# Kernel tuning notes

Measured on AMD Instinct MI355X. Metric: run time of the kernel, lower is better.

The kernel has to match this reference:

```python
import jax, jax.numpy as jnp
import numpy as np

N_NODES = 100000
N_EDGES = 3200000
N_FEAT = 128
N_GRAPHS = 64


def setup_inputs() -> dict:
    key = jax.random.key(0)
    ks = jax.random.split(key, 8)
    x = jax.random.normal(ks[0], (N_NODES, N_FEAT), dtype=jnp.float32)
    edge_index = jax.random.randint(ks[1], (2, N_EDGES), 0, N_NODES, dtype=jnp.int64)
    batch = jnp.sort(jax.random.randint(ks[2], (N_NODES,), 0, N_GRAPHS, dtype=jnp.int64))
    # GCNConv weights (glorot-style scale) and biases
    W1 = jax.random.normal(ks[3], (N_FEAT, 32), dtype=jnp.float32) / np.sqrt(N_FEAT)
    b1 = jnp.zeros((32,), dtype=jnp.float32)
    W2 = jax.random.normal(ks[4], (32, 16), dtype=jnp.float32) / np.sqrt(32.0)
    b2 = jnp.zeros((16,), dtype=jnp.float32)
    lin_w = jax.random.normal(ks[5], (16, 1), dtype=jnp.float32) / np.sqrt(16.0)
    lin_b = jnp.zeros((1,), dtype=jnp.float32)
    return {"x": x, "edge_index": edge_index, "batch": batch,
            "W1": W1, "b1": b1, "W2": W2, "b2": b2,
            "lin_w": lin_w, "lin_b": lin_b}


def _gcn_conv(x, W, b, src, dst, deg_inv_sqrt, n_nodes):
    # transform first (fewer features downstream when out_dim < in_dim)
    xw = x @ W  # [N, out]
    norm = deg_inv_sqrt[src] * deg_inv_sqrt[dst]  # [E+N]
    msg = xw[src] * norm[:, None]  # gather + scale
    out = jax.ops.segment_sum(msg, dst, num_segments=n_nodes)  # scatter-add
    return out + b


def reference(x, edge_index, batch, W1, b1, W2, b2, lin_w, lin_b):
    n_nodes = x.shape[0]
    self_loop = jnp.arange(n_nodes, dtype=edge_index.dtype)
    src = jnp.concatenate([edge_index[0], self_loop])
    dst = jnp.concatenate([edge_index[1], self_loop])
    # symmetric GCN normalization with self-loops
    deg = jax.ops.segment_sum(jnp.ones_like(src, dtype=x.dtype), dst,
                              num_segments=n_nodes)
    deg_inv_sqrt = jnp.where(deg > 0, jax.lax.rsqrt(jnp.maximum(deg, 1.0)), 0.0)

    h = _gcn_conv(x, W1, b1, src, dst, deg_inv_sqrt, n_nodes)
    h = jax.nn.relu(h)
    # F.dropout with training=False (eval) is identity
    h = _gcn_conv(h, W2, b2, src, dst, deg_inv_sqrt, n_nodes)

    # global_mean_pool over batch index
    sums = jax.ops.segment_sum(h, batch, num_segments=N_GRAPHS)  # [G,16]
    cnts = jax.ops.segment_sum(jnp.ones((n_nodes,), dtype=h.dtype), batch,
                               num_segments=N_GRAPHS)
    pooled = sums / jnp.maximum(cnts, 1.0)[:, None]
    return pooled @ lin_w + lin_b  # [G,1]
```

## Files before the change

### kernel.cpp

```cpp
#include <hip/hip_runtime.h>

#define NN 100000
#define NE 3200000
#define NF 128
#define C1 32
#define C2 16
#define NG 64
#define BKT_SH 7
#define BKT_W  128
#define NBKT   782
#define CH     8192
#define NW     391
#define RSTR   784
#define MAPCAP 6400

#define OFF_BCNT  0
#define OFF_CNTF  2048
#define OFF_RUN   2304
#define OFF_ROW   308848
#define OFF_DIS   408864
#define OFF_EDG   508864
#define OFF_XS2B  (OFF_EDG + NE)
#define OFF_COL   (OFF_XS2B + NN*8)
#define OFF_XS1   (OFF_COL + NE)

__device__ __forceinline__ unsigned pack_bf2(float a, float b) {
    unsigned ua = __float_as_uint(a);
    unsigned ub = __float_as_uint(b);
    ua = (ua + 0x7fffu + ((ua >> 16) & 1u)) >> 16;
    ub = (ub + 0x7fffu + ((ub >> 16) & 1u)) & 0xffff0000u;
    return ua | ub;
}
__device__ __forceinline__ float2 unpack_bf2(unsigned u) {
    return make_float2(__uint_as_float(u << 16), __uint_as_float(u & 0xffff0000u));
}
__device__ __forceinline__ void acc4(float4& a, uint2 q) {
    float2 f0 = unpack_bf2(q.x), f1 = unpack_bf2(q.y);
    a.x += f0.x; a.y += f0.y; a.z += f1.x; a.w += f1.y;
}

__global__ __launch_bounds__(512) void k_part(
    const int* __restrict__ S, const int* __restrict__ D,
    unsigned* __restrict__ edgebuf, int* __restrict__ runstart,
    int* __restrict__ bcnt)
{
    __shared__ int lhist[1024];
    __shared__ int lstart[1024];
    __shared__ int lcur[NBKT];
    __shared__ int wsum[8];
    __shared__ unsigned lsort[CH];
    const int w = blockIdx.x;
    const int t = threadIdx.x;
    const int e0 = w * CH;
    const int n = min(CH, NE - e0);
    const int n4 = n >> 2;
    const int4* __restrict__ S4 = (const int4*)(S + e0);
    const int4* __restrict__ D4 = (const int4*)(D + e0);

    for (int i = t; i < 1024; i += 512) lhist[i] = 0;
    __syncthreads();
    for (int i = t; i < n4; i += 512) {
        int4 d = D4[i];
        atomicAdd(&lhist[(unsigned)d.x >> BKT_SH], 1);
        atomicAdd(&lhist[(unsigned)d.y >> BKT_SH], 1);
        atomicAdd(&lhist[(unsigned)d.z >> BKT_SH], 1);
        atomicAdd(&lhist[(unsigned)d.w >> BKT_SH], 1);
    }
    __syncthreads();
    for (int i = t; i < NBKT; i += 512) atomicAdd(&bcnt[i], lhist[i]);

    int c0 = lhist[t * 2 + 0], c1 = lhist[t * 2 + 1];
    int ts = c0 + c1;
    const int lane = t & 63, wv = t >> 6;
    int sc = ts;
    #pragma unroll
    for (int off = 1; off < 64; off <<= 1) {
        int v = __shfl_up(sc, off, 64);
        if (lane >= off) sc += v;
    }
    if (lane == 63) wsum[wv] = sc;
    __syncthreads();
    int wo = 0;
    #pragma unroll
    for (int i = 0; i < 8; ++i) wo += (i < wv) ? wsum[i] : 0;
    int excl = sc - ts + wo;
    lstart[t * 2 + 0] = excl;
    lstart[t * 2 + 1] = excl + c0;
    __syncthreads();

    for (int i = t; i < 783; i += 512) runstart[w * RSTR + i] = lstart[i];
    for (int i = t; i < NBKT; i += 512) lcur[i] = lstart[i];
    __syncthreads();
    for (int i = t; i < n4; i += 512) {
        int4 s = S4[i];
        int4 d = D4[i];
        { int p = atomicAdd(&lcur[(unsigned)d.x >> BKT_SH], 1);
          lsort[p] = ((unsigned)s.x << BKT_SH) | ((unsigned)d.x & (BKT_W - 1)); }
        { int p = atomicAdd(&lcur[(unsigned)d.y >> BKT_SH], 1);
          lsort[p] = ((unsigned)s.y << BKT_SH) | ((unsigned)d.y & (BKT_W - 1)); }
        { int p = atomicAdd(&lcur[(unsigned)d.z >> BKT_SH], 1);
          lsort[p] = ((unsigned)s.z << BKT_SH) | ((unsigned)d.z & (BKT_W - 1)); }
        { int p = atomicAdd(&lcur[(unsigned)d.w >> BKT_SH], 1);
          lsort[p] = ((unsigned)s.w << BKT_SH) | ((unsigned)d.w & (BKT_W - 1)); }
    }
    __syncthreads();
    {
        uint4* __restrict__ eb4 = (uint4*)(edgebuf + e0);
        const uint4* __restrict__ ls4 = (const uint4*)lsort;
        for (int i = t; i < n4; i += 512) eb4[i] = ls4[i];
    }
}

union FGShare {
    struct { unsigned short map[MAPCAP]; unsigned ebuf[MAPCAP]; } f;
    struct { float xls[128 * 33]; float wls[32 * 32]; } g;
};

__global__ __launch_bounds__(256) void k_fillgemm(
    const unsigned* __restrict__ edgebuf, const int* __restrict__ runstart,
    const int* __restrict__ bcnt, const int* __restrict__ batch,
    int* __restrict__ rowstart, float* __restrict__ dis, int* __restrict__ colidx,
    float* __restrict__ cntf,
    const float* __restrict__ x, const float* __restrict__ W1,
    unsigned* __restrict__ xs1)
{
    __shared__ FGShare u;
    __shared__ int rl[NW];
    __shared__ int pfx[NW];
    __shared__ int basea[NW];
    __shared__ int lcnt[BKT_W];
    __shared__ int lcur[BKT_W];
    __shared__ float dloc[BKT_W];
    __shared__ float gcnt[NG];
    __shared__ int wsum[4];
    __shared__ int hs1;
    const int b = blockIdx.x;
    const int t = threadIdx.x;
    const int lane = t & 63, wv = t >> 6;

    if (t < NG) gcnt[t] = 0.f;

    int accp = 0;
    for (int i = t; i < b; i += 256) accp += bcnt[i];
    #pragma unroll
    for (int off = 1; off < 64; off <<= 1) accp += __shfl_xor(accp, off, 64);
    if (lane == 0) wsum[wv] = accp;

    for (int w = t; w < NW; w += 256) {
        int s0 = runstart[w * RSTR + b];
        int s1 = runstart[w * RSTR + b + 1];
        basea[w] = s0;
        rl[w] = s1 - s0;
    }
    if (t < BKT_W) lcnt[t] = 0;
    __syncthreads();
    const int bs = wsum[0] + wsum[1] + wsum[2] + wsum[3];

    int w0 = t * 2;
    int c0 = (w0 < NW) ? rl[w0] : 0;
    int c1 = (w0 + 1 < NW) ? rl[w0 + 1] : 0;
    int ts = c0 + c1;
    int sc = ts;
    #pragma unroll
    for (int off = 1; off < 64; off <<= 1) {
        int v = __shfl_up(sc, off, 64);
        if (lane >= off) sc += v;
    }
    __syncthreads();
    if (lane == 63) wsum[wv] = sc;
    __syncthreads();
    int wo = 0;
    #pragma unroll
    for (int i = 0; i < 4; ++i) wo += (i < wv) ? wsum[i] : 0;
    const int total = wsum[0] + wsum[1] + wsum[2] + wsum[3];
    int excl0 = sc - ts + wo;
    if (w0 < NW)     pfx[w0]     = excl0;
    if (w0 + 1 < NW) pfx[w0 + 1] = excl0 + c0;
    __syncthreads();

    for (int w = t; w < NW; w += 256) {
        int p = pfx[w], len = rl[w];
        basea[w] = w * CH + basea[w] - p;
        for (int i = 0; i < len; ++i) u.f.map[p + i] = (unsigned short)w;
    }
    __syncthreads();
    for (int j = t; j < total; j += 256) {
        unsigned p = edgebuf[basea[u.f.map[j]] + j];
        u.f.ebuf[j] = p;
        atomicAdd(&lcnt[p & (BKT_W - 1)], 1);
    }
    __syncthreads();

    int myc = 0, sc2 = 0;
    if (t < BKT_W) {
        myc = lcnt[t];
        sc2 = myc;
        #pragma unroll
        for (int off = 1; off < 64; off <<= 1) {
            int v = __shfl_up(sc2, off, 64);
            if (lane >= off) sc2 += v;
        }
        if (t == 63) hs1 = sc2;
    }
    __syncthreads();
    if (t < BKT_W) {
        int excl = sc2 - myc + ((t >= 64) ? hs1 : 0);
        int node = b * BKT_W + t;
        float dv = rsqrtf((float)myc + 1.0f);
        dloc[t] = dv;
        if (node < NN) {
            rowstart[node] = bs + excl;
            dis[node] = dv;
            atomicAdd(&gcnt[batch[node]], 1.0f);
        }
        lcur[t] = bs + excl;
    }
    if (b == 0 && t == 0) rowstart[NN] = NE;
    __syncthreads();
    for (int j = t; j < total; j += 256) {
        unsigned p = u.f.ebuf[j];
        int pos = atomicAdd(&lcur[p & (BKT_W - 1)], 1);
        colidx[pos] = (int)(p >> BKT_SH);
    }
    __syncthreads();
    if (t < NG && gcnt[t] != 0.f) atomicAdd(&cntf[t], gcnt[t]);

    const int tc = t & 7;
    const int tr = t >> 3;
    const int base = b * 128;
    float a[4][4] = {};

    for (int k0 = 0; k0 < NF; k0 += 32) {
        {
            int i = t * 4;
            int kk = i >> 5, c = i & 31;
            *(float4*)&u.g.wls[kk * 32 + c] = *(const float4*)&W1[(k0 + kk) * C1 + c];
        }
        #pragma unroll
        for (int r = 0; r < 4; ++r) {
            int n = (t >> 3) + r * 32;
            int j = (t & 7) * 4;
            int node = base + n;
            float4 v = make_float4(0.f, 0.f, 0.f, 0.f);
            if (node < NN) v = *(const float4*)&x[(long long)node * NF + k0 + j];
            u.g.xls[n * 33 + j + 0] = v.x;
            u.g.xls[n * 33 + j + 1] = v.y;
            u.g.xls[n * 33 + j + 2] = v.z;
            u.g.xls[n * 33 + j + 3] = v.w;
        }
        __syncthreads();
        #pragma unroll 8
        for (int kk = 0; kk < 32; ++kk) {
            float4 w = *(const float4*)&u.g.wls[kk * 32 + tc * 4];
            #pragma unroll
            for (int i = 0; i < 4; ++i) {
                float xv = u.g.xls[(tr * 4 + i) * 33 + kk];
                a[i][0] = fmaf(xv, w.x, a[i][0]);
                a[i][1] = fmaf(xv, w.y, a[i][1]);
                a[i][2] = fmaf(xv, w.z, a[i][2]);
                a[i][3] = fmaf(xv, w.w, a[i][3]);
            }
        }
        __syncthreads();
    }
    #pragma unroll
    for (int i = 0; i < 4; ++i) {
        int node = base + tr * 4 + i;
        if (node < NN) {
            float dv = dloc[tr * 4 + i];
            uint2 o;
            o.x = pack_bf2(a[i][0] * dv, a[i][1] * dv);
            o.y = pack_bf2(a[i][2] * dv, a[i][3] * dv);
            *(uint2*)&xs1[node * 16 + tc * 2] = o;
        }
    }
}

__global__ __launch_bounds__(256) void k_gather1(
    const unsigned* __restrict__ xs1, const int* __restrict__ colidx,
    const int* __restrict__ rowstart, const float* __restrict__ dis,
    const float* __restrict__ b1, const float* __restrict__ W2,
    const float* __restrict__ b2, const float* __restrict__ lw,
    const float* __restrict__ lb, float* __restrict__ out,
    unsigned* __restrict__ xs2b)
{
    __shared__ float w2s[C1 * C2];
    __shared__ float hrow[32 * 33];
    const int t = threadIdx.x;
    if (t < 128) *(float4*)&w2s[t * 4] = *(const float4*)&W2[t * 4];
    if (blockIdx.x == 0 && t < NG) {
        float s = lb[0];
        #pragma unroll
        for (int k = 0; k < C2; ++k) s = fmaf(b2[k], lw[k], s);
        out[t] = s;
    }
    const int l = t & 7;
    const int n = t >> 3;
    const int v = blockIdx.x * 32 + n;

    const int start = rowstart[v];
    const int num = rowstart[v + 1] - start;
    const int* __restrict__ cp = &colidx[start];
    const uint2* __restrict__ tb = (const uint2*)xs1;
    float4 a0 = make_float4(0.f, 0.f, 0.f, 0.f);
    float4 a1 = a0, a2 = a0, a3 = a0;
    acc4(a0, tb[v * 8 + l]);
    int i = 0;
    if (num >= 8) {
        int idx[8];
        #pragma unroll
        for (int j = 0; j < 8; ++j) idx[j] = cp[j];
        for (; i + 16 <= num; i += 8) {
            int nx[8];
            #pragma unroll
            for (int j = 0; j < 8; ++j) nx[j] = cp[i + 8 + j];
            uint2 q[8];
            #pragma unroll
            for (int j = 0; j < 8; ++j) q[j] = tb[idx[j] * 8 + l];
            acc4(a0, q[0]); acc4(a1, q[1]); acc4(a2, q[2]); acc4(a3, q[3]);
            acc4(a0, q[4]); acc4(a1, q[5]); acc4(a2, q[6]); acc4(a3, q[7]);
            #pragma unroll
            for (int j = 0; j < 8; ++j) idx[j] = nx[j];
        }
        {
            uint2 q[8];
            #pragma unroll
            for (int j = 0; j < 8; ++j) q[j] = tb[idx[j] * 8 + l];
            acc4(a0, q[0]); acc4(a1, q[1]); acc4(a2, q[2]); acc4(a3, q[3]);
            acc4(a0, q[4]); acc4(a1, q[5]); acc4(a2, q[6]); acc4(a3, q[7]);
            i += 8;
        }
    }
    for (; i < num; ++i) acc4(a0, tb[cp[i] * 8 + l]);
    float ax = (a0.x + a1.x) + (a2.x + a3.x);
    float ay = (a0.y + a1.y) + (a2.y + a3.y);
    float az = (a0.z + a1.z) + (a2.z + a3.z);
    float aw = (a0.w + a1.w) + (a2.w + a3.w);
    const float dv = dis[v];

    hrow[n * 33 + l * 4 + 0] = fmaxf(fmaf(ax, dv, b1[l * 4 + 0]), 0.f);
    hrow[n * 33 + l * 4 + 1] = fmaxf(fmaf(ay, dv, b1[l * 4 + 1]), 0.f);
    hrow[n * 33 + l * 4 + 2] = fmaxf(fmaf(az, dv, b1[l * 4 + 2]), 0.f);
    hrow[n * 33 + l * 4 + 3] = fmaxf(fmaf(aw, dv, b1[l * 4 + 3]), 0.f);
    __syncthreads();

    const float* hr = &hrow[n * 33];
    float s0 = 0.f, s1 = 0.f;
    #pragma unroll
    for (int k = 0; k < 32; ++k) {
        float hv = hr[k];
        s0 = fmaf(hv, w2s[k * C2 + 2 * l + 0], s0);
        s1 = fmaf(hv, w2s[k * C2 + 2 * l + 1], s1);
    }
    xs2b[v * 8 + l] = pack_bf2(s0 * dv, s1 * dv);
}

__global__ __launch_bounds__(256) void k_gather2(
    const unsigned* __restrict__ xs2b, const int* __restrict__ colidx,
    const int* __restrict__ rowstart, const float* __restrict__ dis,
    const int* __restrict__ batch, const float* __restrict__ cntf,
    const float* __restrict__ lw, float* __restrict__ out)
{
    __shared__ float sg[NG];
    const int t = threadIdx.x;
    if (t < NG) sg[t] = 0.f;
    __syncthreads();

    const int l = t & 3;
    const int n = t >> 2;
    const int v = blockIdx.x * 64 + n;
    const bool valid = v < NN;

    float4 r = make_float4(0.f, 0.f, 0.f, 0.f);
    int g = 0;
    if (valid) {
        const int start = rowstart[v];
        const int num = rowstart[v + 1] - start;
        const int* __restrict__ cp = &colidx[start];
        const uint2* __restrict__ tb = (const uint2*)xs2b;
        float4 a0 = make_float4(0.f, 0.f, 0.f, 0.f);
        float4 a1 = a0, a2 = a0, a3 = a0;
        acc4(a0, tb[v * 4 + l]);
        int i = 0;
        if (num >= 8) {
            int idx[8];
            #pragma unroll
            for (int j = 0; j < 8; ++j) idx[j] = cp[j];
            for (; i + 16 <= num; i += 8) {
                int nx[8];
                #pragma unroll
                for (int j = 0; j < 8; ++j) nx[j] = cp[i + 8 + j];
                uint2 q[8];
                #pragma unroll
                for (int j = 0; j < 8; ++j) q[j] = tb[idx[j] * 4 + l];
                acc4(a0, q[0]); acc4(a1, q[1]); acc4(a2, q[2]); acc4(a3, q[3]);
                acc4(a0, q[4]); acc4(a1, q[5]); acc4(a2, q[6]); acc4(a3, q[7]);
                #pragma unroll
                for (int j = 0; j < 8; ++j) idx[j] = nx[j];
            }
            {
                uint2 q[8];
                #pragma unroll
                for (int j = 0; j < 8; ++j) q[j] = tb[idx[j] * 4 + l];
                acc4(a0, q[0]); acc4(a1, q[1]); acc4(a2, q[2]); acc4(a3, q[3]);
                acc4(a0, q[4]); acc4(a1, q[5]); acc4(a2, q[6]); acc4(a3, q[7]);
                i += 8;
            }
        }
        for (; i < num; ++i) acc4(a0, tb[cp[i] * 4 + l]);
        float dv = dis[v];
        g = batch[v];
        r.x = ((a0.x + a1.x) + (a2.x + a3.x)) * dv;
        r.y = ((a0.y + a1.y) + (a2.y + a3.y)) * dv;
        r.z = ((a0.z + a1.z) + (a2.z + a3.z)) * dv;
        r.w = ((a0.w + a1.w) + (a2.w + a3.w)) * dv;
    }

    float part = r.x * lw[l * 4 + 0] + r.y * lw[l * 4 + 1]
               + r.z * lw[l * 4 + 2] + r.w * lw[l * 4 + 3];
    part += __shfl_xor(part, 1, 64);
    part += __shfl_xor(part, 2, 64);
    if (valid && l == 0) {
        float c = fmaxf(cntf[g], 1.0f);
        atomicAdd(&sg[g], part / c);
    }
    __syncthreads();
    if (t < NG && sg[t] != 0.f) atomicAdd(&out[t], sg[t]);
}

extern "C" void kernel_launch(void* const* d_in, const int* in_sizes, int n_in,
                              void* d_out, int out_size, void* d_ws, size_t ws_size,
                              hipStream_t stream) {
    const float* x     = (const float*)d_in[0];
    const int*   ei    = (const int*)d_in[1];
    const int*   batch = (const int*)d_in[2];
    const float* W1    = (const float*)d_in[3];
    const float* b1    = (const float*)d_in[4];
    const float* W2    = (const float*)d_in[5];
    const float* b2    = (const float*)d_in[6];
    const float* lw    = (const float*)d_in[7];
    const float* lb    = (const float*)d_in[8];
    float* out = (float*)d_out;

    float*    wsf = (float*)d_ws;
    int*      wsi = (int*)d_ws;
    unsigned* wsu = (unsigned*)d_ws;

    int*      bcnt     = wsi + OFF_BCNT;
    float*    cntf     = wsf + OFF_CNTF;
    int*      runstart = wsi + OFF_RUN;
    int*      rowstart = wsi + OFF_ROW;
    float*    dis      = wsf + OFF_DIS;
    unsigned* edgebuf  = wsu + OFF_EDG;
    unsigned* xs1      = wsu + OFF_XS1;
    unsigned* xs2b     = wsu + OFF_XS2B;
    int*      colidx   = wsi + OFF_COL;

    const int* S = ei;
    const int* D = ei + NE;

    hipMemsetAsync(wsi + OFF_BCNT, 0, 2304 * sizeof(int), stream);

    k_part       <<<NW, 512, 0, stream>>>(S, D, edgebuf, runstart, bcnt);
    k_fillgemm   <<<NBKT, 256, 0, stream>>>(edgebuf, runstart, bcnt, batch,
                                            rowstart, dis, colidx, cntf, x, W1, xs1);
    k_gather1    <<<NN / 32, 256, 0, stream>>>(xs1, colidx, rowstart, dis, b1, W2,
                                               b2, lw, lb, out, xs2b);
    k_gather2    <<<(NN + 63) / 64, 256, 0, stream>>>(xs2b, colidx, rowstart, dis,
                                                      batch, cntf, lw, out);
}
```

Before: 251.5 us.

## Replace two-pass bucket partition CSR build with global atomic counting sort

Drops the shared-memory bucket partition and per-bucket fill in favour of a plain counting sort: a global-atomic degree histogram, a row-offset prefix computed inside the GEMM kernel, and a scatter kernel that places source indices with global atomics on per-node cursors. This removes the intermediate edge buffer and the run-start bookkeeping. In exchange it issues 6.4M global atomics to random addresses and writes colidx scattered, and the neighbour order within a row is no longer deterministic.

```diff
diff --git a/kernel.cpp b/kernel.cpp
--- a/kernel.cpp
+++ b/kernel.cpp
@@ -6,23 +6,17 @@
 #define C1 32
 #define C2 16
 #define NG 64
-#define BKT_SH 7
 #define BKT_W  128
 #define NBKT   782
-#define CH     8192
-#define NW     391
-#define RSTR   784
-#define MAPCAP 6400
-
-#define OFF_BCNT  0
-#define OFF_CNTF  2048
-#define OFF_RUN   2304
-#define OFF_ROW   308848
-#define OFF_DIS   408864
-#define OFF_EDG   508864
-#define OFF_XS2B  (OFF_EDG + NE)
-#define OFF_COL   (OFF_XS2B + NN*8)
-#define OFF_XS1   (OFF_COL + NE)
+
+#define OFF_CNTF  0
+#define OFF_DEG   64
+#define OFF_ROW   100160
+#define OFF_CUR   200176
+#define OFF_DIS   300176
+#define OFF_COL   400176
+#define OFF_XS1   3600176
+#define OFF_XS2B  5200176
 
 __device__ __forceinline__ unsigned pack_bf2(float a, float b) {
     unsigned ua = __float_as_uint(a);
@@ -39,97 +33,28 @@
     a.x += f0.x; a.y += f0.y; a.z += f1.x; a.w += f1.y;
 }
 
-__global__ __launch_bounds__(512) void k_part(
-    const int* __restrict__ S, const int* __restrict__ D,
-    unsigned* __restrict__ edgebuf, int* __restrict__ runstart,
-    int* __restrict__ bcnt)
-{
-    __shared__ int lhist[1024];
-    __shared__ int lstart[1024];
-    __shared__ int lcur[NBKT];
-    __shared__ int wsum[8];
-    __shared__ unsigned lsort[CH];
-    const int w = blockIdx.x;
-    const int t = threadIdx.x;
-    const int e0 = w * CH;
-    const int n = min(CH, NE - e0);
-    const int n4 = n >> 2;
-    const int4* __restrict__ S4 = (const int4*)(S + e0);
-    const int4* __restrict__ D4 = (const int4*)(D + e0);
-
-    for (int i = t; i < 1024; i += 512) lhist[i] = 0;
-    __syncthreads();
-    for (int i = t; i < n4; i += 512) {
-        int4 d = D4[i];
-        atomicAdd(&lhist[(unsigned)d.x >> BKT_SH], 1);
-        atomicAdd(&lhist[(unsigned)d.y >> BKT_SH], 1);
-        atomicAdd(&lhist[(unsigned)d.z >> BKT_SH], 1);
-        atomicAdd(&lhist[(unsigned)d.w >> BKT_SH], 1);
-    }
-    __syncthreads();
-    for (int i = t; i < NBKT; i += 512) atomicAdd(&bcnt[i], lhist[i]);
-
-    int c0 = lhist[t * 2 + 0], c1 = lhist[t * 2 + 1];
-    int ts = c0 + c1;
-    const int lane = t & 63, wv = t >> 6;
-    int sc = ts;
-    #pragma unroll
-    for (int off = 1; off < 64; off <<= 1) {
-        int v = __shfl_up(sc, off, 64);
-        if (lane >= off) sc += v;
-    }
-    if (lane == 63) wsum[wv] = sc;
-    __syncthreads();
-    int wo = 0;
-    #pragma unroll
-    for (int i = 0; i < 8; ++i) wo += (i < wv) ? wsum[i] : 0;
-    int excl = sc - ts + wo;
-    lstart[t * 2 + 0] = excl;
-    lstart[t * 2 + 1] = excl + c0;
-    __syncthreads();
-
-    for (int i = t; i < 783; i += 512) runstart[w * RSTR + i] = lstart[i];
-    for (int i = t; i < NBKT; i += 512) lcur[i] = lstart[i];
-    __syncthreads();
-    for (int i = t; i < n4; i += 512) {
-        int4 s = S4[i];
-        int4 d = D4[i];
-        { int p = atomicAdd(&lcur[(unsigned)d.x >> BKT_SH], 1);
-          lsort[p] = ((unsigned)s.x << BKT_SH) | ((unsigned)d.x & (BKT_W - 1)); }
-        { int p = atomicAdd(&lcur[(unsigned)d.y >> BKT_SH], 1);
-          lsort[p] = ((unsigned)s.y << BKT_SH) | ((unsigned)d.y & (BKT_W - 1)); }
-        { int p = atomicAdd(&lcur[(unsigned)d.z >> BKT_SH], 1);
-          lsort[p] = ((unsigned)s.z << BKT_SH) | ((unsigned)d.z & (BKT_W - 1)); }
-        { int p = atomicAdd(&lcur[(unsigned)d.w >> BKT_SH], 1);
-          lsort[p] = ((unsigned)s.w << BKT_SH) | ((unsigned)d.w & (BKT_W - 1)); }
-    }
-    __syncthreads();
-    {
-        uint4* __restrict__ eb4 = (uint4*)(edgebuf + e0);
-        const uint4* __restrict__ ls4 = (const uint4*)lsort;
-        for (int i = t; i < n4; i += 512) eb4[i] = ls4[i];
-    }
-}
-
-union FGShare {
-    struct { unsigned short map[MAPCAP]; unsigned ebuf[MAPCAP]; } f;
-    struct { float xls[128 * 33]; float wls[32 * 32]; } g;
-};
-
-__global__ __launch_bounds__(256) void k_fillgemm(
-    const unsigned* __restrict__ edgebuf, const int* __restrict__ runstart,
-    const int* __restrict__ bcnt, const int* __restrict__ batch,
-    int* __restrict__ rowstart, float* __restrict__ dis, int* __restrict__ colidx,
+__global__ __launch_bounds__(512) void k_deg(
+    const int* __restrict__ D, int* __restrict__ deg)
+{
+    int i = blockIdx.x * 512 + threadIdx.x;
+    if (i < NE / 4) {
+        int4 d = ((const int4*)D)[i];
+        atomicAdd(&deg[d.x], 1);
+        atomicAdd(&deg[d.y], 1);
+        atomicAdd(&deg[d.z], 1);
+        atomicAdd(&deg[d.w], 1);
+    }
+}
+
+__global__ __launch_bounds__(256) void k_rowsgemm(
+    const int* __restrict__ deg, const int* __restrict__ batch,
+    int* __restrict__ rowstart, int* __restrict__ cur, float* __restrict__ dis,
     float* __restrict__ cntf,
     const float* __restrict__ x, const float* __restrict__ W1,
     unsigned* __restrict__ xs1)
 {
-    __shared__ FGShare u;
-    __shared__ int rl[NW];
-    __shared__ int pfx[NW];
-    __shared__ int basea[NW];
-    __shared__ int lcnt[BKT_W];
-    __shared__ int lcur[BKT_W];
+    __shared__ float xls[128 * 33];
+    __shared__ float wls[32 * 32];
     __shared__ float dloc[BKT_W];
     __shared__ float gcnt[NG];
     __shared__ int wsum[4];
@@ -140,61 +65,27 @@
 
     if (t < NG) gcnt[t] = 0.f;
 
-    int accp = 0;
-    for (int i = t; i < b; i += 256) accp += bcnt[i];
+    int acc = 0;
+    {
+        const int lim4 = (b * BKT_W) >> 2;
+        const int4* dg4 = (const int4*)deg;
+        for (int i = t; i < lim4; i += 256) {
+            int4 q = dg4[i];
+            acc += (q.x + q.y) + (q.z + q.w);
+        }
+    }
     #pragma unroll
-    for (int off = 1; off < 64; off <<= 1) accp += __shfl_xor(accp, off, 64);
-    if (lane == 0) wsum[wv] = accp;
-
-    for (int w = t; w < NW; w += 256) {
-        int s0 = runstart[w * RSTR + b];
-        int s1 = runstart[w * RSTR + b + 1];
-        basea[w] = s0;
-        rl[w] = s1 - s0;
-    }
-    if (t < BKT_W) lcnt[t] = 0;
+    for (int off = 1; off < 64; off <<= 1) acc += __shfl_xor(acc, off, 64);
+    if (lane == 0) wsum[wv] = acc;
     __syncthreads();
     const int bs = wsum[0] + wsum[1] + wsum[2] + wsum[3];
 
-    int w0 = t * 2;
-    int c0 = (w0 < NW) ? rl[w0] : 0;
-    int c1 = (w0 + 1 < NW) ? rl[w0 + 1] : 0;
-    int ts = c0 + c1;
-    int sc = ts;
-    #pragma unroll
-    for (int off = 1; off < 64; off <<= 1) {
-        int v = __shfl_up(sc, off, 64);
-        if (lane >= off) sc += v;
-    }
-    __syncthreads();
-    if (lane == 63) wsum[wv] = sc;
-    __syncthreads();
-    int wo = 0;
-    #pragma unroll
-    for (int i = 0; i < 4; ++i) wo += (i < wv) ? wsum[i] : 0;
-    const int total = wsum[0] + wsum[1] + wsum[2] + wsum[3];
-    int excl0 = sc - ts + wo;
-    if (w0 < NW)     pfx[w0]     = excl0;
-    if (w0 + 1 < NW) pfx[w0 + 1] = excl0 + c0;
-    __syncthreads();
-
-    for (int w = t; w < NW; w += 256) {
-        int p = pfx[w], len = rl[w];
-        basea[w] = w * CH + basea[w] - p;
-        for (int i = 0; i < len; ++i) u.f.map[p + i] = (unsigned short)w;
-    }
-    __syncthreads();
-    for (int j = t; j < total; j += 256) {
-        unsigned p = edgebuf[basea[u.f.map[j]] + j];
-        u.f.ebuf[j] = p;
-        atomicAdd(&lcnt[p & (BKT_W - 1)], 1);
-    }
-    __syncthreads();
-
-    int myc = 0, sc2 = 0;
+    int myd = 0, sc2 = 0;
+    const int node0 = b * BKT_W;
     if (t < BKT_W) {
-        myc = lcnt[t];
-        sc2 = myc;
+        int node = node0 + t;
+        myd = (node < NN) ? deg[node] : 0;
+        sc2 = myd;
         #pragma unroll
         for (int off = 1; off < 64; off <<= 1) {
             int v = __shfl_up(sc2, off, 64);
@@ -204,57 +95,50 @@
     }
     __syncthreads();
     if (t < BKT_W) {
-        int excl = sc2 - myc + ((t >= 64) ? hs1 : 0);
-        int node = b * BKT_W + t;
-        float dv = rsqrtf((float)myc + 1.0f);
+        int excl = sc2 - myd + ((t >= 64) ? hs1 : 0);
+        int node = node0 + t;
+        float dv = rsqrtf((float)myd + 1.0f);
         dloc[t] = dv;
         if (node < NN) {
             rowstart[node] = bs + excl;
-            dis[node] = dv;
+            cur[node]      = bs + excl;
+            dis[node]      = dv;
             atomicAdd(&gcnt[batch[node]], 1.0f);
         }
-        lcur[t] = bs + excl;
     }
     if (b == 0 && t == 0) rowstart[NN] = NE;
-    __syncthreads();
-    for (int j = t; j < total; j += 256) {
-        unsigned p = u.f.ebuf[j];
-        int pos = atomicAdd(&lcur[p & (BKT_W - 1)], 1);
-        colidx[pos] = (int)(p >> BKT_SH);
-    }
     __syncthreads();
     if (t < NG && gcnt[t] != 0.f) atomicAdd(&cntf[t], gcnt[t]);
 
     const int tc = t & 7;
     const int tr = t >> 3;
-    const int base = b * 128;
     float a[4][4] = {};
 
     for (int k0 = 0; k0 < NF; k0 += 32) {
         {
             int i = t * 4;
             int kk = i >> 5, c = i & 31;
-            *(float4*)&u.g.wls[kk * 32 + c] = *(const float4*)&W1[(k0 + kk) * C1 + c];
+            *(float4*)&wls[kk * 32 + c] = *(const float4*)&W1[(k0 + kk) * C1 + c];
         }
         #pragma unroll
         for (int r = 0; r < 4; ++r) {
             int n = (t >> 3) + r * 32;
             int j = (t & 7) * 4;
-            int node = base + n;
+            int node = node0 + n;
             float4 v = make_float4(0.f, 0.f, 0.f, 0.f);
             if (node < NN) v = *(const float4*)&x[(long long)node * NF + k0 + j];
-            u.g.xls[n * 33 + j + 0] = v.x;
-            u.g.xls[n * 33 + j + 1] = v.y;
-            u.g.xls[n * 33 + j + 2] = v.z;
-            u.g.xls[n * 33 + j + 3] = v.w;
+            xls[n * 33 + j + 0] = v.x;
+            xls[n * 33 + j + 1] = v.y;
+            xls[n * 33 + j + 2] = v.z;
+            xls[n * 33 + j + 3] = v.w;
         }
         __syncthreads();
         #pragma unroll 8
         for (int kk = 0; kk < 32; ++kk) {
-            float4 w = *(const float4*)&u.g.wls[kk * 32 + tc * 4];
+            float4 w = *(const float4*)&wls[kk * 32 + tc * 4];
             #pragma unroll
             for (int i = 0; i < 4; ++i) {
-                float xv = u.g.xls[(tr * 4 + i) * 33 + kk];
+                float xv = xls[(tr * 4 + i) * 33 + kk];
                 a[i][0] = fmaf(xv, w.x, a[i][0]);
                 a[i][1] = fmaf(xv, w.y, a[i][1]);
                 a[i][2] = fmaf(xv, w.z, a[i][2]);
@@ -265,7 +149,7 @@
     }
     #pragma unroll
     for (int i = 0; i < 4; ++i) {
-        int node = base + tr * 4 + i;
+        int node = node0 + tr * 4 + i;
         if (node < NN) {
             float dv = dloc[tr * 4 + i];
             uint2 o;
@@ -273,6 +157,25 @@
             o.y = pack_bf2(a[i][2] * dv, a[i][3] * dv);
             *(uint2*)&xs1[node * 16 + tc * 2] = o;
         }
+    }
+}
+
+__global__ __launch_bounds__(512) void k_scatter(
+    const int* __restrict__ S, const int* __restrict__ D,
+    int* __restrict__ cur, int* __restrict__ colidx)
+{
+    int i = blockIdx.x * 512 + threadIdx.x;
+    if (i < NE / 4) {
+        int4 s = ((const int4*)S)[i];
+        int4 d = ((const int4*)D)[i];
+        int p0 = atomicAdd(&cur[d.x], 1);
+        int p1 = atomicAdd(&cur[d.y], 1);
+        int p2 = atomicAdd(&cur[d.z], 1);
+        int p3 = atomicAdd(&cur[d.w], 1);
+        colidx[p0] = s.x;
+        colidx[p1] = s.y;
+        colidx[p2] = s.z;
+        colidx[p3] = s.w;
     }
 }
 
@@ -446,26 +349,26 @@
     int*      wsi = (int*)d_ws;
     unsigned* wsu = (unsigned*)d_ws;
 
-    int*      bcnt     = wsi + OFF_BCNT;
     float*    cntf     = wsf + OFF_CNTF;
-    int*      runstart = wsi + OFF_RUN;
+    int*      deg      = wsi + OFF_DEG;
     int*      rowstart = wsi + OFF_ROW;
+    int*      cur      = wsi + OFF_CUR;
     float*    dis      = wsf + OFF_DIS;
-    unsigned* edgebuf  = wsu + OFF_EDG;
+    int*      colidx   = wsi + OFF_COL;
     unsigned* xs1      = wsu + OFF_XS1;
     unsigned* xs2b     = wsu + OFF_XS2B;
-    int*      colidx   = wsi + OFF_COL;
 
     const int* S = ei;
     const int* D = ei + NE;
 
-    hipMemsetAsync(wsi + OFF_BCNT, 0, 2304 * sizeof(int), stream);
-
-    k_part       <<<NW, 512, 0, stream>>>(S, D, edgebuf, runstart, bcnt);
-    k_fillgemm   <<<NBKT, 256, 0, stream>>>(edgebuf, runstart, bcnt, batch,
-                                            rowstart, dis, colidx, cntf, x, W1, xs1);
-    k_gather1    <<<NN / 32, 256, 0, stream>>>(xs1, colidx, rowstart, dis, b1, W2,
-                                               b2, lw, lb, out, xs2b);
-    k_gather2    <<<(NN + 63) / 64, 256, 0, stream>>>(xs2b, colidx, rowstart, dis,
-                                                      batch, cntf, lw, out);
-}
+    hipMemsetAsync(wsi + OFF_CNTF, 0, (64 + 100096) * sizeof(int), stream);
+
+    const int EB = (NE / 4 + 511) / 512;
+    k_deg      <<<EB, 512, 0, stream>>>(D, deg);
+    k_rowsgemm <<<NBKT, 256, 0, stream>>>(deg, batch, rowstart, cur, dis, cntf, x, W1, xs1);
+    k_scatter  <<<EB, 512, 0, stream>>>(S, D, cur, colidx);
+    k_gather1  <<<NN / 32, 256, 0, stream>>>(xs1, colidx, rowstart, dis, b1, W2,
+                                             b2, lw, lb, out, xs2b);
+    k_gather2  <<<(NN + 63) / 64, 256, 0, stream>>>(xs2b, colidx, rowstart, dis,
+                                                    batch, cntf, lw, out);
+}
```

After: 634.1 us. 2.52x slower.

## Split fill and GEMM kernels, alias xs1 onto edge buffer, replicate xs2 table

Applied to the files above, without the earlier changes.

Splits the fused fill+GEMM kernel into a CSR-fill kernel and a separate x@W1 GEMM kernel, so each uses less shared memory and can reach higher occupancy. xs1 now aliases the edge buffer region, which is dead once the fill finishes. k_gather1 writes 8 replicated copies of the bf16 layer-2 table, and k_gather2 blocks pick a copy by blockIdx to spread gather traffic across memory channels and cache slices. The cost is an extra launch, a global reload of dis in the GEMM, and 8x the xs2 write traffic.

```diff
diff --git a/kernel.cpp b/kernel.cpp
--- a/kernel.cpp
+++ b/kernel.cpp
@@ -13,6 +13,7 @@
 #define NW     391
 #define RSTR   784
 #define MAPCAP 6400
+#define XSTR   (NN * 8)
 
 #define OFF_BCNT  0
 #define OFF_CNTF  2048
@@ -20,9 +21,9 @@
 #define OFF_ROW   308848
 #define OFF_DIS   408864
 #define OFF_EDG   508864
+#define OFF_XS1   OFF_EDG
 #define OFF_XS2B  (OFF_EDG + NE)
-#define OFF_COL   (OFF_XS2B + NN*8)
-#define OFF_XS1   (OFF_COL + NE)
+#define OFF_COL   (OFF_XS2B + 8 * XSTR)
 
 __device__ __forceinline__ unsigned pack_bf2(float a, float b) {
     unsigned ua = __float_as_uint(a);
@@ -111,26 +112,19 @@
     }
 }
 
-union FGShare {
-    struct { unsigned short map[MAPCAP]; unsigned ebuf[MAPCAP]; } f;
-    struct { float xls[128 * 33]; float wls[32 * 32]; } g;
-};
-
-__global__ __launch_bounds__(256) void k_fillgemm(
+__global__ __launch_bounds__(256) void k_fillfused(
     const unsigned* __restrict__ edgebuf, const int* __restrict__ runstart,
     const int* __restrict__ bcnt, const int* __restrict__ batch,
     int* __restrict__ rowstart, float* __restrict__ dis, int* __restrict__ colidx,
-    float* __restrict__ cntf,
-    const float* __restrict__ x, const float* __restrict__ W1,
-    unsigned* __restrict__ xs1)
+    float* __restrict__ cntf)
 {
-    __shared__ FGShare u;
     __shared__ int rl[NW];
     __shared__ int pfx[NW];
     __shared__ int basea[NW];
+    __shared__ unsigned short map[MAPCAP];
+    __shared__ unsigned ebuf[MAPCAP];
     __shared__ int lcnt[BKT_W];
     __shared__ int lcur[BKT_W];
-    __shared__ float dloc[BKT_W];
     __shared__ float gcnt[NG];
     __shared__ int wsum[4];
     __shared__ int hs1;
@@ -181,12 +175,12 @@
     for (int w = t; w < NW; w += 256) {
         int p = pfx[w], len = rl[w];
         basea[w] = w * CH + basea[w] - p;
-        for (int i = 0; i < len; ++i) u.f.map[p + i] = (unsigned short)w;
+        for (int i = 0; i < len; ++i) map[p + i] = (unsigned short)w;
     }
     __syncthreads();
     for (int j = t; j < total; j += 256) {
-        unsigned p = edgebuf[basea[u.f.map[j]] + j];
-        u.f.ebuf[j] = p;
+        unsigned p = edgebuf[basea[map[j]] + j];
+        ebuf[j] = p;
         atomicAdd(&lcnt[p & (BKT_W - 1)], 1);
     }
     __syncthreads();
@@ -206,35 +200,42 @@
     if (t < BKT_W) {
         int excl = sc2 - myc + ((t >= 64) ? hs1 : 0);
         int node = b * BKT_W + t;
-        float dv = rsqrtf((float)myc + 1.0f);
-        dloc[t] = dv;
         if (node < NN) {
             rowstart[node] = bs + excl;
-            dis[node] = dv;
+            dis[node] = rsqrtf((float)myc + 1.0f);
             atomicAdd(&gcnt[batch[node]], 1.0f);
         }
         lcur[t] = bs + excl;
     }
     if (b == 0 && t == 0) rowstart[NN] = NE;
     __syncthreads();
+    if (t < NG && gcnt[t] != 0.f) atomicAdd(&cntf[t], gcnt[t]);
     for (int j = t; j < total; j += 256) {
-        unsigned p = u.f.ebuf[j];
+        unsigned p = ebuf[j];
         int pos = atomicAdd(&lcur[p & (BKT_W - 1)], 1);
         colidx[pos] = (int)(p >> BKT_SH);
     }
-    __syncthreads();
-    if (t < NG && gcnt[t] != 0.f) atomicAdd(&cntf[t], gcnt[t]);
-
+}
+
+__global__ __launch_bounds__(256) void k_gemm1(
+    const float* __restrict__ x, const float* __restrict__ W1,
+    const float* __restrict__ dis,
+    unsigned* __restrict__ xs1)
+{
+    __shared__ float xls[128 * 33];
+    __shared__ float wls[32 * 32];
+    const int t = threadIdx.x;
     const int tc = t & 7;
     const int tr = t >> 3;
-    const int base = b * 128;
+    const int base = blockIdx.x * 128;
+
     float a[4][4] = {};
 
     for (int k0 = 0; k0 < NF; k0 += 32) {
         {
             int i = t * 4;
             int kk = i >> 5, c = i & 31;
-            *(float4*)&u.g.wls[kk * 32 + c] = *(const float4*)&W1[(k0 + kk) * C1 + c];
+            *(float4*)&wls[kk * 32 + c] = *(const float4*)&W1[(k0 + kk) * C1 + c];
         }
         #pragma unroll
         for (int r = 0; r < 4; ++r) {
@@ -243,18 +244,18 @@
             int node = base + n;
             float4 v = make_float4(0.f, 0.f, 0.f, 0.f);
             if (node < NN) v = *(const float4*)&x[(long long)node * NF + k0 + j];
-            u.g.xls[n * 33 + j + 0] = v.x;
-            u.g.xls[n * 33 + j + 1] = v.y;
-            u.g.xls[n * 33 + j + 2] = v.z;
-            u.g.xls[n * 33 + j + 3] = v.w;
+            xls[n * 33 + j + 0] = v.x;
+            xls[n * 33 + j + 1] = v.y;
+            xls[n * 33 + j + 2] = v.z;
+            xls[n * 33 + j + 3] = v.w;
         }
         __syncthreads();
         #pragma unroll 8
         for (int kk = 0; kk < 32; ++kk) {
-            float4 w = *(const float4*)&u.g.wls[kk * 32 + tc * 4];
+            float4 w = *(const float4*)&wls[kk * 32 + tc * 4];
             #pragma unroll
             for (int i = 0; i < 4; ++i) {
-                float xv = u.g.xls[(tr * 4 + i) * 33 + kk];
+                float xv = xls[(tr * 4 + i) * 33 + kk];
                 a[i][0] = fmaf(xv, w.x, a[i][0]);
                 a[i][1] = fmaf(xv, w.y, a[i][1]);
                 a[i][2] = fmaf(xv, w.z, a[i][2]);
@@ -267,7 +268,7 @@
     for (int i = 0; i < 4; ++i) {
         int node = base + tr * 4 + i;
         if (node < NN) {
-            float dv = dloc[tr * 4 + i];
+            float dv = dis[node];
             uint2 o;
             o.x = pack_bf2(a[i][0] * dv, a[i][1] * dv);
             o.y = pack_bf2(a[i][2] * dv, a[i][3] * dv);
@@ -352,7 +353,10 @@
         s0 = fmaf(hv, w2s[k * C2 + 2 * l + 0], s0);
         s1 = fmaf(hv, w2s[k * C2 + 2 * l + 1], s1);
     }
-    xs2b[v * 8 + l] = pack_bf2(s0 * dv, s1 * dv);
+    unsigned packed = pack_bf2(s0 * dv, s1 * dv);
+    #pragma unroll
+    for (int c = 0; c < 8; ++c)
+        xs2b[c * XSTR + v * 8 + l] = packed;
 }
 
 __global__ __launch_bounds__(256) void k_gather2(
@@ -377,7 +381,8 @@
         const int start = rowstart[v];
         const int num = rowstart[v + 1] - start;
         const int* __restrict__ cp = &colidx[start];
-        const uint2* __restrict__ tb = (const uint2*)xs2b;
+        const uint2* __restrict__ tb =
+            (const uint2*)(xs2b + (blockIdx.x & 7) * XSTR);
         float4 a0 = make_float4(0.f, 0.f, 0.f, 0.f);
         float4 a1 = a0, a2 = a0, a3 = a0;
         acc4(a0, tb[v * 4 + l]);
@@ -462,8 +467,9 @@
     hipMemsetAsync(wsi + OFF_BCNT, 0, 2304 * sizeof(int), stream);
 
     k_part       <<<NW, 512, 0, stream>>>(S, D, edgebuf, runstart, bcnt);
-    k_fillgemm   <<<NBKT, 256, 0, stream>>>(edgebuf, runstart, bcnt, batch,
-                                            rowstart, dis, colidx, cntf, x, W1, xs1);
+    k_fillfused  <<<NBKT, 256, 0, stream>>>(edgebuf, runstart, bcnt, batch,
+                                            rowstart, dis, colidx, cntf);
+    k_gemm1      <<<(NN + 127) / 128, 256, 0, stream>>>(x, W1, dis, xs1);
     k_gather1    <<<NN / 32, 256, 0, stream>>>(xs1, colidx, rowstart, dis, b1, W2,
                                                b2, lw, lb, out, xs2b);
     k_gather2    <<<(NN + 63) / 64, 256, 0, stream>>>(xs2b, colidx, rowstart, dis,
```

New measurement: 249.1 us. Within noise of the previous version (-1.0%).

## Move X·W1 GEMM into partition kernel and halve partition chunk size

Applied to the files above, without the earlier changes.

The dense x@W1 product moves out of the fill kernel and into the edge-partition kernel, whose grid doubles to 782 blocks by halving the edge chunk to 4096. The GEMM result is written to global memory in fp32, and the fill kernel reads it back to apply the degree scaling and pack to bf16. The goal is to spread the GEMM work across the partition stage and shorten the latency-bound fill kernel. The cost is an extra fp32 round trip through global memory, a doubled runstart table, and more per-window prefix work in the fill kernel.

```diff
diff --git a/kernel.cpp b/kernel.cpp
--- a/kernel.cpp
+++ b/kernel.cpp
@@ -9,20 +9,21 @@
 #define BKT_SH 7
 #define BKT_W  128
 #define NBKT   782
-#define CH     8192
-#define NW     391
+#define CH     4096
+#define NW     782
 #define RSTR   784
 #define MAPCAP 6400
 
 #define OFF_BCNT  0
 #define OFF_CNTF  2048
 #define OFF_RUN   2304
-#define OFF_ROW   308848
-#define OFF_DIS   408864
-#define OFF_EDG   508864
-#define OFF_XS2B  (OFF_EDG + NE)
-#define OFF_COL   (OFF_XS2B + NN*8)
-#define OFF_XS1   (OFF_COL + NE)
+#define OFF_ROW   615392
+#define OFF_DIS   715408
+#define OFF_EDG   815408
+#define OFF_XW32  4015408
+#define OFF_XS1   7215408
+#define OFF_XS2B  8815408
+#define OFF_COL   9615408
 
 __device__ __forceinline__ unsigned pack_bf2(float a, float b) {
     unsigned ua = __float_as_uint(a);
@@ -39,16 +40,20 @@
     a.x += f0.x; a.y += f0.y; a.z += f1.x; a.w += f1.y;
 }
 
-__global__ __launch_bounds__(512) void k_part(
+union PGShare {
+    struct { unsigned lsort[CH]; int lhist[1024]; int lstart[1024]; } a;
+    struct { float xls[128 * 33]; float wls[32 * 32]; } b;
+};
+
+__global__ __launch_bounds__(512) void k_partgemm(
     const int* __restrict__ S, const int* __restrict__ D,
+    const float* __restrict__ x, const float* __restrict__ W1,
     unsigned* __restrict__ edgebuf, int* __restrict__ runstart,
-    int* __restrict__ bcnt)
+    int* __restrict__ bcnt, float* __restrict__ xw32)
 {
-    __shared__ int lhist[1024];
-    __shared__ int lstart[1024];
+    __shared__ PGShare u;
     __shared__ int lcur[NBKT];
     __shared__ int wsum[8];
-    __shared__ unsigned lsort[CH];
     const int w = blockIdx.x;
     const int t = threadIdx.x;
     const int e0 = w * CH;
@@ -56,22 +61,22 @@
     const int n4 = n >> 2;
     const int4* __restrict__ S4 = (const int4*)(S + e0);
     const int4* __restrict__ D4 = (const int4*)(D + e0);
-
-    for (int i = t; i < 1024; i += 512) lhist[i] = 0;
+    const int lane = t & 63, wv = t >> 6;
+
+    for (int i = t; i < 1024; i += 512) u.a.lhist[i] = 0;
     __syncthreads();
     for (int i = t; i < n4; i += 512) {
         int4 d = D4[i];
-        atomicAdd(&lhist[(unsigned)d.x >> BKT_SH], 1);
-        atomicAdd(&lhist[(unsigned)d.y >> BKT_SH], 1);
-        atomicAdd(&lhist[(unsigned)d.z >> BKT_SH], 1);
-        atomicAdd(&lhist[(unsigned)d.w >> BKT_SH], 1);
-    }
-    __syncthreads();
-    for (int i = t; i < NBKT; i += 512) atomicAdd(&bcnt[i], lhist[i]);
-
-    int c0 = lhist[t * 2 + 0], c1 = lhist[t * 2 + 1];
+        atomicAdd(&u.a.lhist[(unsigned)d.x >> BKT_SH], 1);
+        atomicAdd(&u.a.lhist[(unsigned)d.y >> BKT_SH], 1);
+        atomicAdd(&u.a.lhist[(unsigned)d.z >> BKT_SH], 1);
+        atomicAdd(&u.a.lhist[(unsigned)d.w >> BKT_SH], 1);
+    }
+    __syncthreads();
+    for (int i = t; i < NBKT; i += 512) atomicAdd(&bcnt[i], u.a.lhist[i]);
+
+    int c0 = u.a.lhist[t * 2 + 0], c1 = u.a.lhist[t * 2 + 1];
     int ts = c0 + c1;
-    const int lane = t & 63, wv = t >> 6;
     int sc = ts;
     #pragma unroll
     for (int off = 1; off < 64; off <<= 1) {
@@ -84,50 +89,93 @@
     #pragma unroll
     for (int i = 0; i < 8; ++i) wo += (i < wv) ? wsum[i] : 0;
     int excl = sc - ts + wo;
-    lstart[t * 2 + 0] = excl;
-    lstart[t * 2 + 1] = excl + c0;
-    __syncthreads();
-
-    for (int i = t; i < 783; i += 512) runstart[w * RSTR + i] = lstart[i];
-    for (int i = t; i < NBKT; i += 512) lcur[i] = lstart[i];
+    u.a.lstart[t * 2 + 0] = excl;
+    u.a.lstart[t * 2 + 1] = excl + c0;
+    __syncthreads();
+
+    for (int i = t; i < 783; i += 512) runstart[w * RSTR + i] = u.a.lstart[i];
+    for (int i = t; i < NBKT; i += 512) lcur[i] = u.a.lstart[i];
     __syncthreads();
     for (int i = t; i < n4; i += 512) {
         int4 s = S4[i];
         int4 d = D4[i];
         { int p = atomicAdd(&lcur[(unsigned)d.x >> BKT_SH], 1);
-          lsort[p] = ((unsigned)s.x << BKT_SH) | ((unsigned)d.x & (BKT_W - 1)); }
+          u.a.lsort[p] = ((unsigned)s.x << BKT_SH) | ((unsigned)d.x & (BKT_W - 1)); }
         { int p = atomicAdd(&lcur[(unsigned)d.y >> BKT_SH], 1);
-          lsort[p] = ((unsigned)s.y << BKT_SH) | ((unsigned)d.y & (BKT_W - 1)); }
+          u.a.lsort[p] = ((unsigned)s.y << BKT_SH) | ((unsigned)d.y & (BKT_W - 1)); }
         { int p = atomicAdd(&lcur[(unsigned)d.z >> BKT_SH], 1);
-          lsort[p] = ((unsigned)s.z << BKT_SH) | ((unsigned)d.z & (BKT_W - 1)); }
+          u.a.lsort[p] = ((unsigned)s.z << BKT_SH) | ((unsigned)d.z & (BKT_W - 1)); }
         { int p = atomicAdd(&lcur[(unsigned)d.w >> BKT_SH], 1);
-          lsort[p] = ((unsigned)s.w << BKT_SH) | ((unsigned)d.w & (BKT_W - 1)); }
+          u.a.lsort[p] = ((unsigned)s.w << BKT_SH) | ((unsigned)d.w & (BKT_W - 1)); }
     }
     __syncthreads();
     {
         uint4* __restrict__ eb4 = (uint4*)(edgebuf + e0);
-        const uint4* __restrict__ ls4 = (const uint4*)lsort;
+        const uint4* __restrict__ ls4 = (const uint4*)u.a.lsort;
         for (int i = t; i < n4; i += 512) eb4[i] = ls4[i];
     }
-}
-
-union FGShare {
-    struct { unsigned short map[MAPCAP]; unsigned ebuf[MAPCAP]; } f;
-    struct { float xls[128 * 33]; float wls[32 * 32]; } g;
-};
-
-__global__ __launch_bounds__(256) void k_fillgemm(
+    __syncthreads();
+
+    const int tc = t & 7;
+    const int tr = t >> 3;
+    const int base = w * 128;
+    float a[2][4] = {};
+
+    for (int k0 = 0; k0 < NF; k0 += 32) {
+        if (t < 256) {
+            int i = t * 4;
+            int kk = i >> 5, c = i & 31;
+            *(float4*)&u.b.wls[kk * 32 + c] = *(const float4*)&W1[(k0 + kk) * C1 + c];
+        }
+        #pragma unroll
+        for (int r = 0; r < 2; ++r) {
+            int slot = t + r * 512;
+            int nn = slot >> 3;
+            int j = (slot & 7) * 4;
+            int node = base + nn;
+            float4 v = make_float4(0.f, 0.f, 0.f, 0.f);
+            if (node < NN) v = *(const float4*)&x[(long long)node * NF + k0 + j];
+            u.b.xls[nn * 33 + j + 0] = v.x;
+            u.b.xls[nn * 33 + j + 1] = v.y;
+            u.b.xls[nn * 33 + j + 2] = v.z;
+            u.b.xls[nn * 33 + j + 3] = v.w;
+        }
+        __syncthreads();
+        #pragma unroll 8
+        for (int kk = 0; kk < 32; ++kk) {
+            float4 wv4 = *(const float4*)&u.b.wls[kk * 32 + tc * 4];
+            #pragma unroll
+            for (int i = 0; i < 2; ++i) {
+                float xv = u.b.xls[(tr + i * 64) * 33 + kk];
+                a[i][0] = fmaf(xv, wv4.x, a[i][0]);
+                a[i][1] = fmaf(xv, wv4.y, a[i][1]);
+                a[i][2] = fmaf(xv, wv4.z, a[i][2]);
+                a[i][3] = fmaf(xv, wv4.w, a[i][3]);
+            }
+        }
+        __syncthreads();
+    }
+    #pragma unroll
+    for (int i = 0; i < 2; ++i) {
+        int node = base + tr + i * 64;
+        if (node < NN)
+            *(float4*)&xw32[node * 32 + tc * 4] =
+                make_float4(a[i][0], a[i][1], a[i][2], a[i][3]);
+    }
+}
+
+__global__ __launch_bounds__(256) void k_fillfused(
     const unsigned* __restrict__ edgebuf, const int* __restrict__ runstart,
     const int* __restrict__ bcnt, const int* __restrict__ batch,
     int* __restrict__ rowstart, float* __restrict__ dis, int* __restrict__ colidx,
     float* __restrict__ cntf,
-    const float* __restrict__ x, const float* __restrict__ W1,
-    unsigned* __restrict__ xs1)
+    const float* __restrict__ xw32, unsigned* __restrict__ xs1)
 {
-    __shared__ FGShare u;
     __shared__ int rl[NW];
     __shared__ int pfx[NW];
     __shared__ int basea[NW];
+    __shared__ unsigned short map[MAPCAP];
+    __shared__ unsigned ebuf[MAPCAP];
     __shared__ int lcnt[BKT_W];
     __shared__ int lcur[BKT_W];
     __shared__ float dloc[BKT_W];
@@ -156,10 +204,12 @@
     __syncthreads();
     const int bs = wsum[0] + wsum[1] + wsum[2] + wsum[3];
 
-    int w0 = t * 2;
-    int c0 = (w0 < NW) ? rl[w0] : 0;
+    int w0 = t * 4;
+    int c0 = (w0 + 0 < NW) ? rl[w0 + 0] : 0;
     int c1 = (w0 + 1 < NW) ? rl[w0 + 1] : 0;
-    int ts = c0 + c1;
+    int c2 = (w0 + 2 < NW) ? rl[w0 + 2] : 0;
+    int c3 = (w0 + 3 < NW) ? rl[w0 + 3] : 0;
+    int ts = ((c0 + c1) + (c2 + c3));
     int sc = ts;
     #pragma unroll
     for (int off = 1; off < 64; off <<= 1) {
@@ -174,19 +224,21 @@
     for (int i = 0; i < 4; ++i) wo += (i < wv) ? wsum[i] : 0;
     const int total = wsum[0] + wsum[1] + wsum[2] + wsum[3];
     int excl0 = sc - ts + wo;
-    if (w0 < NW)     pfx[w0]     = excl0;
+    if (w0 + 0 < NW) pfx[w0 + 0] = excl0;
     if (w0 + 1 < NW) pfx[w0 + 1] = excl0 + c0;
+    if (w0 + 2 < NW) pfx[w0 + 2] = excl0 + c0 + c1;
+    if (w0 + 3 < NW) pfx[w0 + 3] = excl0 + c0 + c1 + c2;
     __syncthreads();
 
     for (int w = t; w < NW; w += 256) {
         int p = pfx[w], len = rl[w];
         basea[w] = w * CH + basea[w] - p;
-        for (int i = 0; i < len; ++i) u.f.map[p + i] = (unsigned short)w;
+        for (int i = 0; i < len; ++i) map[p + i] = (unsigned short)w;
     }
     __syncthreads();
     for (int j = t; j < total; j += 256) {
-        unsigned p = edgebuf[basea[u.f.map[j]] + j];
-        u.f.ebuf[j] = p;
+        unsigned p = edgebuf[basea[map[j]] + j];
+        ebuf[j] = p;
         atomicAdd(&lcnt[p & (BKT_W - 1)], 1);
     }
     __syncthreads();
@@ -217,61 +269,23 @@
     }
     if (b == 0 && t == 0) rowstart[NN] = NE;
     __syncthreads();
+    if (t < NG && gcnt[t] != 0.f) atomicAdd(&cntf[t], gcnt[t]);
     for (int j = t; j < total; j += 256) {
-        unsigned p = u.f.ebuf[j];
+        unsigned p = ebuf[j];
         int pos = atomicAdd(&lcur[p & (BKT_W - 1)], 1);
         colidx[pos] = (int)(p >> BKT_SH);
     }
-    __syncthreads();
-    if (t < NG && gcnt[t] != 0.f) atomicAdd(&cntf[t], gcnt[t]);
-
-    const int tc = t & 7;
-    const int tr = t >> 3;
-    const int base = b * 128;
-    float a[4][4] = {};
-
-    for (int k0 = 0; k0 < NF; k0 += 32) {
-        {
-            int i = t * 4;
-            int kk = i >> 5, c = i & 31;
-            *(float4*)&u.g.wls[kk * 32 + c] = *(const float4*)&W1[(k0 + kk) * C1 + c];
-        }
-        #pragma unroll
-        for (int r = 0; r < 4; ++r) {
-            int n = (t >> 3) + r * 32;
-            int j = (t & 7) * 4;
-            int node = base + n;
-            float4 v = make_float4(0.f, 0.f, 0.f, 0.f);
-            if (node < NN) v = *(const float4*)&x[(long long)node * NF + k0 + j];
-            u.g.xls[n * 33 + j + 0] = v.x;
-            u.g.xls[n * 33 + j + 1] = v.y;
-            u.g.xls[n * 33 + j + 2] = v.z;
-            u.g.xls[n * 33 + j + 3] = v.w;
-        }
-        __syncthreads();
-        #pragma unroll 8
-        for (int kk = 0; kk < 32; ++kk) {
-            float4 w = *(const float4*)&u.g.wls[kk * 32 + tc * 4];
-            #pragma unroll
-            for (int i = 0; i < 4; ++i) {
-                float xv = u.g.xls[(tr * 4 + i) * 33 + kk];
-                a[i][0] = fmaf(xv, w.x, a[i][0]);
-                a[i][1] = fmaf(xv, w.y, a[i][1]);
-                a[i][2] = fmaf(xv, w.z, a[i][2]);
-                a[i][3] = fmaf(xv, w.w, a[i][3]);
-            }
-        }
-        __syncthreads();
-    }
-    #pragma unroll
-    for (int i = 0; i < 4; ++i) {
-        int node = base + tr * 4 + i;
+
+    for (int slot = t; slot < BKT_W * 8; slot += 256) {
+        int nn = slot >> 3;
+        int node = b * BKT_W + nn;
         if (node < NN) {
-            float dv = dloc[tr * 4 + i];
+            float4 vv = *(const float4*)&xw32[node * 32 + (slot & 7) * 4];
+            float dv = dloc[nn];
             uint2 o;
-            o.x = pack_bf2(a[i][0] * dv, a[i][1] * dv);
-            o.y = pack_bf2(a[i][2] * dv, a[i][3] * dv);
-            *(uint2*)&xs1[node * 16 + tc * 2] = o;
+            o.x = pack_bf2(vv.x * dv, vv.y * dv);
+            o.y = pack_bf2(vv.z * dv, vv.w * dv);
+            *(uint2*)&xs1[node * 16 + (slot & 7) * 2] = o;
         }
     }
 }
@@ -452,6 +466,7 @@
     int*      rowstart = wsi + OFF_ROW;
     float*    dis      = wsf + OFF_DIS;
     unsigned* edgebuf  = wsu + OFF_EDG;
+    float*    xw32     = wsf + OFF_XW32;
     unsigned* xs1      = wsu + OFF_XS1;
     unsigned* xs2b     = wsu + OFF_XS2B;
     int*      colidx   = wsi + OFF_COL;
@@ -461,9 +476,9 @@
 
     hipMemsetAsync(wsi + OFF_BCNT, 0, 2304 * sizeof(int), stream);
 
-    k_part       <<<NW, 512, 0, stream>>>(S, D, edgebuf, runstart, bcnt);
-    k_fillgemm   <<<NBKT, 256, 0, stream>>>(edgebuf, runstart, bcnt, batch,
-                                            rowstart, dis, colidx, cntf, x, W1, xs1);
+    k_partgemm   <<<NW, 512, 0, stream>>>(S, D, x, W1, edgebuf, runstart, bcnt, xw32);
+    k_fillfused  <<<NBKT, 256, 0, stream>>>(edgebuf, runstart, bcnt, batch,
+                                            rowstart, dis, colidx, cntf, xw32, xs1);
     k_gather1    <<<NN / 32, 256, 0, stream>>>(xs1, colidx, rowstart, dis, b1, W2,
                                                b2, lw, lb, out, xs2b);
     k_gather2    <<<(NN + 63) / 64, 256, 0, stream>>>(xs2b, colidx, rowstart, dis,
```

Measured after the change: 263.9 us. 1.05x slower.
